# Performance work log

Measured on AMD Instinct MI355X. Metric: run time of the kernel, lower is better.

Reference implementation:

```python
import jax, jax.numpy as jnp
import numpy as np

B, T, K, H = 4, 2048, 128, 8
MASK = True


def setup_inputs() -> dict:
    key = jax.random.key(0)
    ks = jax.random.split(key, 6)
    s = 0.02
    return {
        "x": jax.random.normal(ks[0], (B, T, K), dtype=jnp.float32),
        "Wq": jax.random.normal(ks[1], (K, H * K), dtype=jnp.float32) * s,
        "Wk": jax.random.normal(ks[2], (K, H * K), dtype=jnp.float32) * s,
        "Wv": jax.random.normal(ks[3], (K, H * K), dtype=jnp.float32) * s,
        "Wu": jax.random.normal(ks[4], (H * K, K), dtype=jnp.float32) * s,
        "bu": jnp.zeros((K,), dtype=jnp.float32),
    }


def reference(x, Wq, Wk, Wv, Wu, bu):
    b, t, k = x.shape
    h = H
    q = (x @ Wq).reshape(b, t, h, k)
    kk = (x @ Wk).reshape(b, t, h, k)
    # module pre-scales values by k**-0.25 (idiosyncratic but faithful)
    v = (x @ Wv).reshape(b, t, h, k) * (k ** -0.25)
    # scores [b, h, t, t], scaled by k**-0.5
    scores = jnp.einsum('bthd,bshd->bhts', q, kk) * (k ** -0.5)
    if MASK:
        causal = jnp.tril(jnp.ones((t, t), dtype=bool))
        scores = jnp.where(causal, scores, -jnp.inf)
    w = jax.nn.softmax(scores, axis=-1)
    out = jnp.einsum('bhts,bshd->bthd', w, v).reshape(b, t, h * k)
    return out @ Wu + bu
```

## Files before the change

### kernel.cpp

```cpp
#include <hip/hip_runtime.h>
#include <hip/hip_bf16.h>
#include <math.h>

#define B_ 4
#define T_ 2048
#define D_ 128
#define H_ 8
#define BT_ 8192
#define HD_ 1024

typedef __attribute__((ext_vector_type(8))) short bf16x8;
typedef __attribute__((ext_vector_type(4))) float f32x4;

__device__ __forceinline__ short f2bf(float f) {
  union { float f; unsigned u; } v; v.f = f;
  return (short)((v.u + 0x8000u) >> 16);
}

#if __has_builtin(__builtin_amdgcn_exp2f)
#define EXP2F(x) __builtin_amdgcn_exp2f(x)
#else
#define EXP2F(x) exp2f(x)
#endif

#define QSCALE 0.12752040242046492f
#define VSCALE 0.29730177875068026f

__device__ __forceinline__ void gld16(const short* g, short* l) {
  __builtin_amdgcn_global_load_lds(
      (const __attribute__((address_space(1))) void*)g,
      (__attribute__((address_space(3))) void*)l, 16, 0, 0);
}

__device__ __forceinline__ void wu_transpose_body(
    const float* __restrict__ Wu, short* __restrict__ WuT,
    short* Tt, int kc, int tid)
{
  #pragma unroll 4
  for (int i = tid; i < 4096; i += 256) {
    int kl = i >> 5, n4 = (i & 31) << 2;
    float4 v = *(const float4*)&Wu[(size_t)(kc*128 + kl) * D_ + n4];
    float vv[4] = {v.x, v.y, v.z, v.w};
    #pragma unroll
    for (int j = 0; j < 4; j++) {
      int n = n4 + j;
      Tt[n*128 + (((kl >> 3) ^ (n & 15)) << 3) + (kl & 7)] = f2bf(vv[j]);
    }
  }
  __syncthreads();
  short* dst = WuT + (size_t)kc * 16384;
  #pragma unroll 2
  for (int i = tid; i < 2048; i += 256)
    *(bf16x8*)&dst[i*8] = *(bf16x8*)&Tt[i*8];
}

__global__ __launch_bounds__(256) void prep(
    const float* __restrict__ x, const float* __restrict__ Wq,
    const float* __restrict__ Wk, const float* __restrict__ Wv,
    const float* __restrict__ Wu,
    short* __restrict__ xbf, short* __restrict__ WT, short* __restrict__ WuT)
{
  __shared__ __align__(16) short Tt[128*128];
  const int tid = threadIdx.x;
  const int id = blockIdx.x;
  if (id < 24) {
    const int wsel = id >> 3, nt = id & 7;
    const float* W = (wsel == 0) ? Wq : (wsel == 1) ? Wk : Wv;
    #pragma unroll 4
    for (int i = tid; i < 4096; i += 256) {
      int k = i >> 5, n4 = (i & 31) << 2;
      float4 v = *(const float4*)&W[(size_t)k * HD_ + nt*128 + n4];
      float vv[4] = {v.x, v.y, v.z, v.w};
      #pragma unroll
      for (int j = 0; j < 4; j++) {
        int n = n4 + j;
        Tt[n*128 + (((k >> 3) ^ (n & 15)) << 3) + (k & 7)] = f2bf(vv[j]);
      }
    }
    __syncthreads();
    short* dst = WT + (size_t)id * 16384;
    #pragma unroll 2
    for (int i = tid; i < 2048; i += 256)
      *(bf16x8*)&dst[i*8] = *(bf16x8*)&Tt[i*8];
  } else if (id < 88) {
    const int xb = id - 24;
    const float* xs = x + (size_t)xb * 16384;
    short* dst = xbf + (size_t)xb * 16384;
    #pragma unroll 4
    for (int i = tid; i < 4096; i += 256) {
      float4 v = ((const float4*)xs)[i];
      int row = i >> 5, c = (i & 31) >> 1, half = i & 1;
      short4 p;
      p.x = f2bf(v.x); p.y = f2bf(v.y); p.z = f2bf(v.z); p.w = f2bf(v.w);
      *(short4*)&dst[(row*16 + (c ^ (row & 15)))*8 + half*4] = p;
    }
  } else {
    wu_transpose_body(Wu, WuT, Tt, id - 88, tid);
  }
}

__global__ __launch_bounds__(256, 3) void qkv_proj(
    const short* __restrict__ xbf, const short* __restrict__ WT,
    short* __restrict__ Qw, short* __restrict__ Kw, short* __restrict__ Vw)
{
  __shared__ __align__(16) short As[8192];
  __shared__ __align__(16) short Bs[16384];
  const int tid = threadIdx.x;
  const int w = tid >> 6, lane = tid & 63, quad = lane >> 4, l16 = lane & 15;
  const int mt = (int)blockIdx.x;
  const int m0 = mt * 64;
  const int head = (int)blockIdx.y;
  const int soA = w*2048 + lane*8;
  const int soB = w*4096 + lane*8;

  {
    const short* asrc = xbf + (size_t)(mt >> 1)*16384 + (size_t)(mt & 1)*8192;
    const short* bsrc = WT + (size_t)head * 16384;
    #pragma unroll
    for (int cc = 0; cc < 4; cc++)
      gld16(asrc + soA + cc*512, &As[w*2048 + cc*512]);
    #pragma unroll
    for (int cc = 0; cc < 8; cc++)
      gld16(bsrc + soB + cc*512, &Bs[w*4096 + cc*512]);
  }

  const int b = m0 >> 11, t0g = m0 & 2047;
  const int h = head;

  #pragma unroll 1
  for (int wsel = 0; wsel < 3; wsel++) {
    __syncthreads();

    if (wsel <= 1) {
      const int rA0 = (w & 1) * 64, rB0 = (w >> 1) * 32;
      f32x4 acc[4][2];
      #pragma unroll
      for (int a = 0; a < 4; a++) {
        acc[a][0] = (f32x4){0.f,0.f,0.f,0.f};
        acc[a][1] = (f32x4){0.f,0.f,0.f,0.f};
      }
      #pragma unroll
      for (int kk = 0; kk < 4; kk++) {
        const int swz = ((kk*4 + quad) ^ l16) << 3;
        bf16x8 af[4], bfv[2];
        #pragma unroll
        for (int ai = 0; ai < 4; ai++) af[ai]  = *(const bf16x8*)&Bs[(rA0 + ai*16 + l16)*128 + swz];
        #pragma unroll
        for (int bi = 0; bi < 2; bi++) bfv[bi] = *(const bf16x8*)&As[(rB0 + bi*16 + l16)*128 + swz];
        #pragma unroll
        for (int ai = 0; ai < 4; ai++)
          #pragma unroll
          for (int bi = 0; bi < 2; bi++)
            acc[ai][bi] = __builtin_amdgcn_mfma_f32_16x16x32_bf16(af[ai], bfv[bi], acc[ai][bi], 0, 0, 0);
      }
      __syncthreads();
      const float sc = wsel ? 1.0f : QSCALE;
      #pragma unroll
      for (int ai = 0; ai < 4; ai++) {
        #pragma unroll
        for (int bi = 0; bi < 2; bi++) {
          const int d0 = rA0 + ai*16 + quad*4;
          const int t  = rB0 + bi*16 + l16;
          short4 p;
          p.x = f2bf(acc[ai][bi][0] * sc);
          p.y = f2bf(acc[ai][bi][1] * sc);
          p.z = f2bf(acc[ai][bi][2] * sc);
          p.w = f2bf(acc[ai][bi][3] * sc);
          *(short4*)&Bs[t*128 + (((d0 >> 3) ^ (t & 15)) << 3) + (d0 & 7)] = p;
        }
      }
    } else {
      const int rA0 = (w & 1) * 32, rB0 = (w >> 1) * 64;
      f32x4 acc[2][4];
      #pragma unroll
      for (int a = 0; a < 2; a++)
        #pragma unroll
        for (int bb = 0; bb < 4; bb++) acc[a][bb] = (f32x4){0.f,0.f,0.f,0.f};
      #pragma unroll
      for (int kk = 0; kk < 4; kk++) {
        const int swz = ((kk*4 + quad) ^ l16) << 3;
        bf16x8 af[2], bfv[4];
        #pragma unroll
        for (int ai = 0; ai < 2; ai++) af[ai]  = *(const bf16x8*)&As[(rA0 + ai*16 + l16)*128 + swz];
        #pragma unroll
        for (int bi = 0; bi < 4; bi++) bfv[bi] = *(const bf16x8*)&Bs[(rB0 + bi*16 + l16)*128 + swz];
        #pragma unroll
        for (int ai = 0; ai < 2; ai++)
          #pragma unroll
          for (int bi = 0; bi < 4; bi++)
            acc[ai][bi] = __builtin_amdgcn_mfma_f32_16x16x32_bf16(af[ai], bfv[bi], acc[ai][bi], 0, 0, 0);
      }
      __syncthreads();
      #pragma unroll
      for (int ai = 0; ai < 2; ai++) {
        #pragma unroll
        for (int bi = 0; bi < 4; bi++) {
          const int t0 = rA0 + ai*16 + quad*4;
          const int d  = rB0 + bi*16 + l16;
          short4 p;
          p.x = f2bf(acc[ai][bi][0] * VSCALE);
          p.y = f2bf(acc[ai][bi][1] * VSCALE);
          p.z = f2bf(acc[ai][bi][2] * VSCALE);
          p.w = f2bf(acc[ai][bi][3] * VSCALE);
          *(short4*)&Bs[d*64 + (((t0 >> 3) ^ (d & 7)) << 3) + (t0 & 7)] = p;
        }
      }
    }
    __syncthreads();

    short* base = ((wsel == 0) ? Qw : (wsel == 1) ? Kw : Vw)
                + (size_t)(b*H_ + h)*262144 + (size_t)t0g*128;
    #pragma unroll 2
    for (int i = tid; i < 1024; i += 256)
      *(bf16x8*)&base[i*8] = *(bf16x8*)&Bs[i*8];

    if (wsel < 2) {
      __syncthreads();
      const short* bsrc = WT + (size_t)((wsel + 1)*8 + head) * 16384;
      #pragma unroll
      for (int cc = 0; cc < 8; cc++)
        gld16(bsrc + soB + cc*512, &Bs[w*4096 + cc*512]);
    }
  }
}

__global__ __launch_bounds__(256, 4) void attn_kernel(
    const short* __restrict__ Qw, const short* __restrict__ Kw,
    const short* __restrict__ Vw, short* __restrict__ attnw)
{
  __shared__ __align__(16) short Ks[8192];
  __shared__ __align__(16) short Vs[8192];
  __shared__ __align__(16) short Ps[4096];

  const int tid = threadIdx.x;
  const int id = (int)blockIdx.x;
  const int xcd = id & 7;
  const int j   = id >> 3;
  const int u   = j & 3;
  const int q   = (j >> 2) & 7;
  const int vv  = (j >> 5) & 3;
  const int slot = u ^ vv;
  const int qi = (slot == 0) ? q : (slot == 1) ? 15 - q
               : (slot == 2) ? 16 + q : 31 - q;
  const int bh = xcd | (u << 3);
  const int b = bh >> 3, h = bh & 7;
  const int w = tid >> 6, lane = tid & 63, quad = lane >> 4, l16 = lane & 15;
  const int rowQ = qi*64 + w*16;

  const short* Qp = Qw + (size_t)bh * 262144;
  const short* Kp = Kw + (size_t)bh * 262144;
  const short* Vp = Vw + (size_t)bh * 262144;

  bf16x8 qa[4];
  {
    const int tl = (rowQ & 63) + l16;
    const short* qp = Qp + ((size_t)(rowQ >> 6) << 13) + tl*128;
    #pragma unroll
    for (int kk = 0; kk < 4; kk++)
      qa[kk] = *(const bf16x8*)(qp + (((kk*4 + quad) ^ (tl & 15)) << 3));
  }

  f32x4 o[4][2];
  #pragma unroll
  for (int m = 0; m < 4; m++) {
    o[m][0] = (f32x4){0,0,0,0};
    o[m][1] = (f32x4){0,0,0,0};
  }
  float l[4] = {0,0,0,0};

  short* Pw = &Ps[w*1024];
  const int so = w*2048 + lane*8;
  const int nIter = qi + 1;

  for (int it = 0; it < nIter; ++it) {
    if (it) __syncthreads();
    {
      const short* kt = Kp + ((size_t)it << 13);
      const short* vt = Vp + ((size_t)it << 13);
      #pragma unroll
      for (int cc = 0; cc < 4; cc++) {
        gld16(kt + so + cc*512, &Ks[w*2048 + cc*512]);
        gld16(vt + so + cc*512, &Vs[w*2048 + cc*512]);
      }
    }
    __syncthreads();

    f32x4 s[4];
    #pragma unroll
    for (int nj = 0; nj < 4; nj++) s[nj] = (f32x4){0,0,0,0};
    __builtin_amdgcn_s_setprio(1);
    #pragma unroll
    for (int kk = 0; kk < 4; kk++) {
      const int swz = ((kk*4 + quad) ^ l16) << 3;
      #pragma unroll
      for (int nj = 0; nj < 4; nj++) {
        bf16x8 kb = *(const bf16x8*)&Ks[(nj*16 + l16)*128 + swz];
        s[nj] = __builtin_amdgcn_mfma_f32_16x16x32_bf16(qa[kk], kb, s[nj], 0, 0, 0);
      }
    }
    __builtin_amdgcn_s_setprio(0);

    if (it < qi) {
      #pragma unroll
      for (int nj = 0; nj < 4; nj++) {
        #pragma unroll
        for (int r = 0; r < 4; r++) {
          float p = EXP2F(s[nj][r]);
          l[r] += p;
          const int row = quad*4 + r, col = nj*16 + l16;
          Pw[row*64 + (((col >> 3) ^ (row & 7)) << 3) + (col & 7)] = f2bf(p);
        }
      }
    } else {
      const int s0 = it * 64;
      #pragma unroll
      for (int nj = 0; nj < 4; nj++) {
        const int key = s0 + nj*16 + l16;
        #pragma unroll
        for (int r = 0; r < 4; r++) {
          float p = (key > rowQ + quad*4 + r) ? 0.f : EXP2F(s[nj][r]);
          l[r] += p;
          const int row = quad*4 + r, col = nj*16 + l16;
          Pw[row*64 + (((col >> 3) ^ (row & 7)) << 3) + (col & 7)] = f2bf(p);
        }
      }
    }
    __syncthreads();

    __builtin_amdgcn_s_setprio(1);
    #pragma unroll
    for (int kk2 = 0; kk2 < 2; kk2++) {
      const int sl = ((kk2*4 + quad) ^ (l16 & 7)) << 3;
      bf16x8 vb0 = *(const bf16x8*)&Vs[(w*32 + l16)*64 + sl];
      bf16x8 vb1 = *(const bf16x8*)&Vs[(w*32 + 16 + l16)*64 + sl];
      #pragma unroll
      for (int m = 0; m < 4; m++) {
        bf16x8 pa = *(const bf16x8*)&Ps[(m*16 + l16)*64 + sl];
        o[m][0] = __builtin_amdgcn_mfma_f32_16x16x32_bf16(pa, vb0, o[m][0], 0, 0, 0);
        o[m][1] = __builtin_amdgcn_mfma_f32_16x16x32_bf16(pa, vb1, o[m][1], 0, 0, 0);
      }
    }
    __builtin_amdgcn_s_setprio(0);
  }

  #pragma unroll
  for (int r = 0; r < 4; r++) {
    float t = l[r];
    t += __shfl_xor(t, 1); t += __shfl_xor(t, 2);
    t += __shfl_xor(t, 4); t += __shfl_xor(t, 8);
    l[r] = 1.0f / t;
  }
  __syncthreads();
  float* Lf = (float*)Ps;
  if (l16 == 0) {
    #pragma unroll
    for (int r = 0; r < 4; r++)
      Lf[w*16 + quad*4 + r] = l[r];
  }
  __syncthreads();
  #pragma unroll
  for (int m = 0; m < 4; m++) {
    #pragma unroll
    for (int dt = 0; dt < 2; dt++) {
      const int col = w*32 + dt*16 + l16;
      const int c = col >> 3;
      #pragma unroll
      for (int r = 0; r < 4; r++) {
        const int row = m*16 + quad*4 + r;
        const int sub = row >> 5, r32 = row & 31;
        Ks[sub*4096 + r32*128 + ((c ^ (r32 & 15)) << 3) + (col & 7)] =
            f2bf(o[m][dt][r] * Lf[row]);
      }
    }
  }
  __syncthreads();
  const int st0 = b*64 + qi*2;
  #pragma unroll 2
  for (int i = tid; i < 1024; i += 256) {
    const int sub = i >> 9, rem = i & 511;
    short* dst = attnw + ((size_t)(st0 + sub)*8 + h)*4096 + rem*8;
    *(bf16x8*)dst = *(const bf16x8*)&Ks[i*8];
  }
}

__global__ __launch_bounds__(256) void wu_prep(
    const float* __restrict__ Wu, short* __restrict__ WuT)
{
  __shared__ __align__(16) short Tt[128*128];
  wu_transpose_body(Wu, WuT, Tt, blockIdx.x, threadIdx.x);
}

__global__ __launch_bounds__(256, 2) void out_proj(
    const short* __restrict__ attnw, const short* __restrict__ WuT,
    const float* __restrict__ bu, float* __restrict__ out)
{
  __shared__ __align__(16) short As2[2][2048];
  __shared__ __align__(16) short Bs2[2][16384];
  const int tid = threadIdx.x;
  const int w = tid >> 6, lane = tid & 63, quad = lane >> 4, l16 = lane & 15;
  const int m0 = (int)blockIdx.x * 16;
  const int mtile32 = m0 >> 5, half = (m0 >> 4) & 1;

  f32x4 o2[2];
  o2[0] = (f32x4){0,0,0,0}; o2[1] = (f32x4){0,0,0,0};

  {
    const short* ab = attnw + (size_t)(mtile32*8)*4096 + half*2048;
    gld16(ab + w*512 + lane*8, &As2[0][w*512]);
    #pragma unroll
    for (int cc = 0; cc < 8; cc++)
      gld16(WuT + w*4096 + cc*512 + lane*8, &Bs2[0][w*4096 + cc*512]);
  }
  int buf = 0;

  for (int kc = 0; kc < 8; kc++) {
    __syncthreads();
    if (kc < 7) {
      const short* ab = attnw + (size_t)(mtile32*8 + kc + 1)*4096 + half*2048;
      const short* bb = WuT + (size_t)(kc + 1)*16384;
      gld16(ab + w*512 + lane*8, &As2[buf^1][w*512]);
      #pragma unroll
      for (int cc = 0; cc < 8; cc++)
        gld16(bb + w*4096 + cc*512 + lane*8, &Bs2[buf^1][w*4096 + cc*512]);
    }
    const short* as = &As2[buf][0];
    const short* bs = &Bs2[buf][0];
    #pragma unroll
    for (int kk = 0; kk < 4; kk++) {
      const int swz = ((kk*4 + quad) ^ l16) << 3;
      bf16x8 a = *(const bf16x8*)&as[l16*128 + swz];
      #pragma unroll
      for (int e = 0; e < 2; e++) {
        bf16x8 bfr = *(const bf16x8*)&bs[((w*2 + e)*16 + l16)*128 + swz];
        o2[e] = __builtin_amdgcn_mfma_f32_16x16x32_bf16(a, bfr, o2[e], 0, 0, 0);
      }
    }
    buf ^= 1;
  }

  #pragma unroll
  for (int e = 0; e < 2; e++) {
    const int n = (w*2 + e)*16 + l16;
    const float bias = bu[n];
    #pragma unroll
    for (int r = 0; r < 4; r++) {
      const int mm = m0 + quad*4 + r;
      out[(size_t)mm*D_ + n] = o2[e][r] + bias;
    }
  }
}

extern "C" void kernel_launch(void* const* d_in, const int* in_sizes, int n_in,
                              void* d_out, int out_size, void* d_ws, size_t ws_size,
                              hipStream_t stream) {
  (void)in_sizes; (void)n_in; (void)out_size;
  const float* x  = (const float*)d_in[0];
  const float* Wq = (const float*)d_in[1];
  const float* Wk = (const float*)d_in[2];
  const float* Wv = (const float*)d_in[3];
  const float* Wu = (const float*)d_in[4];
  const float* bu = (const float*)d_in[5];
  float* out = (float*)d_out;

  const size_t headElems = (size_t)B_ * H_ * T_ * D_;
  short* Qw    = (short*)d_ws;
  short* Kw    = Qw + headElems;
  short* Vw    = Kw + headElems;
  short* attnw = Vw + headElems;
  short* xbf = attnw;
  short* WT  = attnw + 1048576;

  const bool extraWu = ws_size >= (64ull << 20) + (1ull << 20);
  short* WuT = extraWu ? (short*)((char*)d_ws + (64ull << 20)) : Kw;

  prep<<<dim3(extraWu ? 96 : 88), 256, 0, stream>>>(x, Wq, Wk, Wv, Wu, xbf, WT, WuT);
  qkv_proj<<<dim3(128, 8), 256, 0, stream>>>(xbf, WT, Qw, Kw, Vw);
  attn_kernel<<<dim3(1024), 256, 0, stream>>>(Qw, Kw, Vw, attnw);
  if (!extraWu) wu_prep<<<dim3(8), 256, 0, stream>>>(Wu, WuT);
  out_proj<<<dim3(512), 256, 0, stream>>>(attnw, WuT, bu, out);
}
```

Baseline: 152.9 us.

## Fuse fp32-to-bf16 conversion of x and weights into QKV projection kernel

```diff
diff --git a/kernel.cpp b/kernel.cpp
--- a/kernel.cpp
+++ b/kernel.cpp
@@ -54,75 +54,55 @@
     *(bf16x8*)&dst[i*8] = *(bf16x8*)&Tt[i*8];
 }
 
-__global__ __launch_bounds__(256) void prep(
+__device__ __forceinline__ void conv_w_tile(
+    const float* __restrict__ W, int head, short* __restrict__ Bs, int tid)
+{
+  #pragma unroll 4
+  for (int i = tid; i < 4096; i += 256) {
+    int k = i >> 5, n4 = (i & 31) << 2;
+    float4 v = *(const float4*)&W[(size_t)k * HD_ + head*128 + n4];
+    float vv[4] = {v.x, v.y, v.z, v.w};
+    #pragma unroll
+    for (int jj = 0; jj < 4; jj++) {
+      int n = n4 + jj;
+      Bs[n*128 + (((k >> 3) ^ (n & 15)) << 3) + (k & 7)] = f2bf(vv[jj]);
+    }
+  }
+}
+
+__global__ __launch_bounds__(256, 3) void qkv_fused(
     const float* __restrict__ x, const float* __restrict__ Wq,
     const float* __restrict__ Wk, const float* __restrict__ Wv,
     const float* __restrict__ Wu,
-    short* __restrict__ xbf, short* __restrict__ WT, short* __restrict__ WuT)
-{
-  __shared__ __align__(16) short Tt[128*128];
+    short* __restrict__ Qw, short* __restrict__ Kw, short* __restrict__ Vw,
+    short* __restrict__ WuT, int doWu)
+{
+  __shared__ __align__(16) short As[8192];
+  __shared__ __align__(16) short Bs[16384];
   const int tid = threadIdx.x;
-  const int id = blockIdx.x;
-  if (id < 24) {
-    const int wsel = id >> 3, nt = id & 7;
-    const float* W = (wsel == 0) ? Wq : (wsel == 1) ? Wk : Wv;
-    #pragma unroll 4
-    for (int i = tid; i < 4096; i += 256) {
-      int k = i >> 5, n4 = (i & 31) << 2;
-      float4 v = *(const float4*)&W[(size_t)k * HD_ + nt*128 + n4];
-      float vv[4] = {v.x, v.y, v.z, v.w};
-      #pragma unroll
-      for (int j = 0; j < 4; j++) {
-        int n = n4 + j;
-        Tt[n*128 + (((k >> 3) ^ (n & 15)) << 3) + (k & 7)] = f2bf(vv[j]);
-      }
-    }
-    __syncthreads();
-    short* dst = WT + (size_t)id * 16384;
+  const int mt = (int)blockIdx.x;
+  const int head = (int)blockIdx.y;
+
+  if (mt == 128) {
+    if (doWu) wu_transpose_body(Wu, WuT, Bs, head, tid);
+    return;
+  }
+
+  const int w = tid >> 6, lane = tid & 63, quad = lane >> 4, l16 = lane & 15;
+  const int m0 = mt * 64;
+
+  {
+    const float* xs = x + (size_t)m0 * D_;
     #pragma unroll 2
-    for (int i = tid; i < 2048; i += 256)
-      *(bf16x8*)&dst[i*8] = *(bf16x8*)&Tt[i*8];
-  } else if (id < 88) {
-    const int xb = id - 24;
-    const float* xs = x + (size_t)xb * 16384;
-    short* dst = xbf + (size_t)xb * 16384;
-    #pragma unroll 4
-    for (int i = tid; i < 4096; i += 256) {
+    for (int i = tid; i < 2048; i += 256) {
       float4 v = ((const float4*)xs)[i];
       int row = i >> 5, c = (i & 31) >> 1, half = i & 1;
       short4 p;
       p.x = f2bf(v.x); p.y = f2bf(v.y); p.z = f2bf(v.z); p.w = f2bf(v.w);
-      *(short4*)&dst[(row*16 + (c ^ (row & 15)))*8 + half*4] = p;
-    }
-  } else {
-    wu_transpose_body(Wu, WuT, Tt, id - 88, tid);
-  }
-}
-
-__global__ __launch_bounds__(256, 3) void qkv_proj(
-    const short* __restrict__ xbf, const short* __restrict__ WT,
-    short* __restrict__ Qw, short* __restrict__ Kw, short* __restrict__ Vw)
-{
-  __shared__ __align__(16) short As[8192];
-  __shared__ __align__(16) short Bs[16384];
-  const int tid = threadIdx.x;
-  const int w = tid >> 6, lane = tid & 63, quad = lane >> 4, l16 = lane & 15;
-  const int mt = (int)blockIdx.x;
-  const int m0 = mt * 64;
-  const int head = (int)blockIdx.y;
-  const int soA = w*2048 + lane*8;
-  const int soB = w*4096 + lane*8;
-
-  {
-    const short* asrc = xbf + (size_t)(mt >> 1)*16384 + (size_t)(mt & 1)*8192;
-    const short* bsrc = WT + (size_t)head * 16384;
-    #pragma unroll
-    for (int cc = 0; cc < 4; cc++)
-      gld16(asrc + soA + cc*512, &As[w*2048 + cc*512]);
-    #pragma unroll
-    for (int cc = 0; cc < 8; cc++)
-      gld16(bsrc + soB + cc*512, &Bs[w*4096 + cc*512]);
-  }
+      *(short4*)&As[(row*16 + (c ^ (row & 15)))*8 + half*4] = p;
+    }
+  }
+  conv_w_tile(Wq, head, Bs, tid);
 
   const int b = m0 >> 11, t0g = m0 & 2047;
   const int h = head;
@@ -216,10 +196,7 @@
 
     if (wsel < 2) {
       __syncthreads();
-      const short* bsrc = WT + (size_t)((wsel + 1)*8 + head) * 16384;
-      #pragma unroll
-      for (int cc = 0; cc < 8; cc++)
-        gld16(bsrc + soB + cc*512, &Bs[w*4096 + cc*512]);
+      conv_w_tile((wsel == 0) ? Wk : Wv, head, Bs, tid);
     }
   }
 }
@@ -467,14 +444,12 @@
   short* Kw    = Qw + headElems;
   short* Vw    = Kw + headElems;
   short* attnw = Vw + headElems;
-  short* xbf = attnw;
-  short* WT  = attnw + 1048576;
 
   const bool extraWu = ws_size >= (64ull << 20) + (1ull << 20);
   short* WuT = extraWu ? (short*)((char*)d_ws + (64ull << 20)) : Kw;
 
-  prep<<<dim3(extraWu ? 96 : 88), 256, 0, stream>>>(x, Wq, Wk, Wv, Wu, xbf, WT, WuT);
-  qkv_proj<<<dim3(128, 8), 256, 0, stream>>>(xbf, WT, Qw, Kw, Vw);
+  qkv_fused<<<dim3(129, 8), 256, 0, stream>>>(x, Wq, Wk, Wv, Wu,
+                                              Qw, Kw, Vw, WuT, (int)extraWu);
   attn_kernel<<<dim3(1024), 256, 0, stream>>>(Qw, Kw, Vw, attnw);
   if (!extraWu) wu_prep<<<dim3(8), 256, 0, stream>>>(Wu, WuT);
   out_proj<<<dim3(512), 256, 0, stream>>>(attnw, WuT, bu, out);
```

Result: slower. 195.1 us (+27.6%).
